# Performance work log

Measured on AMD Instinct MI355X. Metric: run time of the kernel, lower is better.

The kernel has to match this reference:

```python
import jax, jax.numpy as jnp
import numpy as np

N_EXPERTS = 32
TOPK = 256
DMODEL = 1024
EXPERT_SIZE = 2048
BATCH = 2
CUTOFF = 4096


def setup_inputs() -> dict:
    key = jax.random.key(0)
    k1, k2, k3, k4 = jax.random.split(key, 4)
    x = jax.random.normal(k1, (BATCH, CUTOFF, DMODEL), dtype=jnp.float32)
    # init scales ~ 1/sqrt(fan_in), mimicking get_init_weight
    gate = jax.random.normal(k2, (CUTOFF, N_EXPERTS), dtype=jnp.float32) / np.sqrt(DMODEL)
    lin1_weight = jax.random.normal(k3, (N_EXPERTS, DMODEL, EXPERT_SIZE), dtype=jnp.float32) / np.sqrt(DMODEL)
    lin2_weight = jax.random.normal(k4, (N_EXPERTS, EXPERT_SIZE, DMODEL), dtype=jnp.float32) / np.sqrt(EXPERT_SIZE)
    return {"x": x, "gate": gate, "lin1_weight": lin1_weight, "lin2_weight": lin2_weight}


def reference(x, gate, lin1_weight, lin2_weight):
    batch_size, cutoff, dmodel = x.shape
    n_experts = lin1_weight.shape[0]
    # gate scores: (batch, cutoff, n_experts) -> (n_experts, batch*cutoff)
    gate_out = jnp.einsum('bcd,ce->bce', x, gate)
    gate_out = jnp.transpose(gate_out, (2, 0, 1)).reshape(n_experts, batch_size * cutoff)
    probs = jax.nn.softmax(gate_out, axis=1)
    # top-k token selection per expert (computed but, faithfully to the original,
    # not used to gather tokens -- the original reshapes tokens contiguously)
    topk_values, topk_indices = jax.lax.top_k(probs, TOPK)
    # contiguous token -> expert grouping (as in the original reshape)
    xe = x.reshape(n_experts, TOPK, dmodel)  # requires batch*cutoff == n_experts*topk
    h = jax.nn.relu(jnp.einsum('ekd,eds->eks', xe, lin1_weight))
    out = jnp.einsum('eks,esd->ekd', h, lin2_weight)
    return out.reshape(batch_size, cutoff, dmodel)
```

## Files before the change

### kernel.cpp

```cpp
#include <hip/hip_runtime.h>
#include <hip/hip_bf16.h>

#define NE 32
#define MM 256
#define DM 1024
#define ES 2048

typedef __attribute__((ext_vector_type(8))) short short8;
typedef __attribute__((ext_vector_type(4))) float f32x4;
typedef unsigned int uint32;
typedef unsigned long long u64;
typedef unsigned short u16;

__device__ __forceinline__ uint32 cvt_pk_bf16(float a, float b) {
    uint32 r;
    asm("v_cvt_pk_bf16_f32 %0, %1, %2" : "=v"(r) : "v"(a), "v"(b));
    return r;
}
__device__ __forceinline__ u64 pack4(float a, float b, float c, float d) {
    return (u64)cvt_pk_bf16(a, b) | ((u64)cvt_pk_bf16(c, d) << 32);
}

__device__ __forceinline__ void gl_lds16(const void* g, void* l) {
    __builtin_amdgcn_global_load_lds(
        (const __attribute__((address_space(1))) uint32*)g,
        (__attribute__((address_space(3))) uint32*)l, 16, 0, 0);
}

__device__ __forceinline__ int b_off(int n, int k) {
    int X = ((n >> 2) & 7) ^ ((n & 3) << 1);
    return n * 128 + ((((k >> 3) ^ X) & 7) << 4) + (((k >> 2) & 1) << 3);
}

__global__ __launch_bounds__(256) void cvt_bf16(const float* __restrict__ x,
                                                u16* __restrict__ xb, int n4) {
    int i = blockIdx.x * blockDim.x + threadIdx.x;
    int stride = gridDim.x * blockDim.x;
    for (; i < n4; i += stride) {
        float4 v = ((const float4*)x)[i];
        ((u64*)xb)[i] = pack4(v.x, v.y, v.z, v.w);
    }
}

template<int N, int K, bool RELU, typename CT>
__global__ __launch_bounds__(256) void ec_gemm(
    const u16* __restrict__ A,
    const float* __restrict__ B,
    CT* __restrict__ C)
{
    constexpr int BM = 128, BN = 128, BK = 64;
    constexpr int MT = MM / BM;
    constexpr int NT = N / BN;
    constexpr int NSTEP = K / BK;
    constexpr int NP  = NE * MT;
    constexpr int PPX = NP / 8;

    int bid   = blockIdx.x;
    int xcd   = bid & 7;
    int local = bid >> 3;
    int p     = xcd * PPX + local / NT;
    int nt    = local % NT;
    int e     = p >> 1;
    int mt    = p & 1;

    const u16*   Ae = A + (size_t)(e * MM + mt * BM) * K;
    const float* Be = B + (size_t)e * K * N + (size_t)nt * BN;
    CT*          Ce = C + (size_t)(e * MM + mt * BM) * N + (size_t)nt * BN;

    __shared__ char AsB[2][BM * BK * 2];
    __shared__ char BsB[2][BN * BK * 2];

    const int t    = threadIdx.x;
    const int lane = t & 63;
    const int w    = t >> 6;
    const int wm   = (w >> 1) * 64;
    const int wn   = (w & 1) * 64;
    const int lr   = lane & 15;
    const int lg   = lane >> 4;

    const int bn4 = (t & 31) * 4;
    const int bkb = (t >> 5) * 4;

    f32x4  acc[4][4] = {};
    float4 br[2][4];

    auto gloadA = [&](int kt, int buf) {
        #pragma unroll
        for (int r = 0; r < 4; ++r) {
            int reg = w * 4 + r;
            int m   = reg * 8 + (lane >> 3);
            int s   = (lane & 7) ^ (m & 7);
            const u16* g = Ae + (size_t)m * K + kt + s * 8;
            gl_lds16(g, AsB[buf] + reg * 1024);
        }
    };
    auto loadB = [&](int kt) {
        #pragma unroll
        for (int g = 0; g < 2; ++g) {
            int k4 = g * 32 + bkb;
            const float* Bk = Be + (size_t)(kt + k4) * N + bn4;
            br[g][0] = *(const float4*)(Bk);
            br[g][1] = *(const float4*)(Bk + N);
            br[g][2] = *(const float4*)(Bk + 2 * (size_t)N);
            br[g][3] = *(const float4*)(Bk + 3 * (size_t)N);
        }
    };
    auto writeB = [&](int buf) {
        #pragma unroll
        for (int g = 0; g < 2; ++g) {
            int k4 = g * 32 + bkb;
            *(u64*)(BsB[buf] + b_off(bn4 + 0, k4)) = pack4(br[g][0].x, br[g][1].x, br[g][2].x, br[g][3].x);
            *(u64*)(BsB[buf] + b_off(bn4 + 1, k4)) = pack4(br[g][0].y, br[g][1].y, br[g][2].y, br[g][3].y);
            *(u64*)(BsB[buf] + b_off(bn4 + 2, k4)) = pack4(br[g][0].z, br[g][1].z, br[g][2].z, br[g][3].z);
            *(u64*)(BsB[buf] + b_off(bn4 + 3, k4)) = pack4(br[g][0].w, br[g][1].w, br[g][2].w, br[g][3].w);
        }
    };
    auto readA = [&](int i, int k, int buf) -> short8 {
        int m = wm + i * 16 + lr;
        int s = ((k >> 3) ^ (m & 7)) & 7;
        return *(const short8*)(AsB[buf] + m * 128 + s * 16);
    };

    loadB(0);
    gloadA(0, 0);
    writeB(0);
    __syncthreads();

    for (int ks = 0; ks < NSTEP; ++ks) {
        const int  c  = ks & 1;
        const bool pf = (ks + 1 < NSTEP);
        if (pf) { gloadA((ks + 1) * BK, c ^ 1); loadB((ks + 1) * BK); }

        #pragma unroll
        for (int kk = 0; kk < 2; ++kk) {
            int k = kk * 32 + lg * 8;
            short8 af[4], bfr[4];
            #pragma unroll
            for (int i = 0; i < 4; ++i) af[i] = readA(i, k, c);
            #pragma unroll
            for (int j = 0; j < 4; ++j)
                bfr[j] = *(const short8*)(BsB[c] + b_off(wn + j * 16 + lr, k));
            #pragma unroll
            for (int i = 0; i < 4; ++i)
                #pragma unroll
                for (int j = 0; j < 4; ++j)
                    acc[i][j] = __builtin_amdgcn_mfma_f32_16x16x32_bf16(af[i], bfr[j], acc[i][j], 0, 0, 0);
        }
        if (pf) writeB(c ^ 1);
        __syncthreads();
    }

    #pragma unroll
    for (int i = 0; i < 4; ++i) {
        #pragma unroll
        for (int rr = 0; rr < 4; ++rr) {
            int row = wm + i * 16 + lg * 4 + rr;
            CT* Cp = Ce + (size_t)row * N + wn + lr;
            if constexpr (sizeof(CT) == 2) {
                #pragma unroll
                for (int jp = 0; jp < 2; ++jp) {
                    float v0 = acc[i][2 * jp + 0][rr];
                    float v1 = acc[i][2 * jp + 1][rr];
                    if constexpr (RELU) {
                        v0 = v0 > 0.0f ? v0 : 0.0f;
                        v1 = v1 > 0.0f ? v1 : 0.0f;
                    }
                    uint32 pk = cvt_pk_bf16(v0, v1);
                    ((u16*)Cp)[(2 * jp + 0) * 16] = (u16)(pk & 0xffffu);
                    ((u16*)Cp)[(2 * jp + 1) * 16] = (u16)(pk >> 16);
                }
            } else {
                #pragma unroll
                for (int j = 0; j < 4; ++j) {
                    float v = acc[i][j][rr];
                    if constexpr (RELU) v = v > 0.0f ? v : 0.0f;
                    ((float*)Cp)[j * 16] = v;
                }
            }
        }
    }
}

extern "C" void kernel_launch(void* const* d_in, const int* in_sizes, int n_in,
                              void* d_out, int out_size, void* d_ws, size_t ws_size,
                              hipStream_t stream) {
    const float* x    = (const float*)d_in[0];
    const float* lin1 = (const float*)d_in[2];
    const float* lin2 = (const float*)d_in[3];
    float* out = (float*)d_out;

    u16* h  = (u16*)d_ws;
    u16* xb = (u16*)((char*)d_ws + (size_t)36 * 1024 * 1024);

    dim3 blk(256);
    cvt_bf16<<<2048, blk, 0, stream>>>(x, xb, NE * MM * DM / 4);
    ec_gemm<ES, DM, true,  u16  ><<<NE * (MM/128) * (ES/128), blk, 0, stream>>>(xb, lin1, h);
    ec_gemm<DM, ES, false, float><<<NE * (MM/128) * (DM/128), blk, 0, stream>>>(h, lin2, out);
}
```

Before: 181.4 us.

## Cover each expert's full 256-token tile per block so weights are read once

The GEMM block tile grows from 128 to 256 rows and 512 threads, so one workgroup covers all 256 tokens of an expert for a given column tile. Each fp32 weight tile is then loaded from global memory and converted to bf16 once instead of twice. This cuts weight traffic and conversion work, which likely dominate this bandwidth-bound kernel. In exchange it doubles LDS use for A, halves the number of blocks, and gives each thread one B row-group per k-step.

```diff
diff --git a/kernel.cpp b/kernel.cpp
--- a/kernel.cpp
+++ b/kernel.cpp
@@ -43,29 +43,25 @@
 }
 
 template<int N, int K, bool RELU, typename CT>
-__global__ __launch_bounds__(256) void ec_gemm(
+__global__ __launch_bounds__(512) void ec_gemm(
     const u16* __restrict__ A,
     const float* __restrict__ B,
     CT* __restrict__ C)
 {
-    constexpr int BM = 128, BN = 128, BK = 64;
-    constexpr int MT = MM / BM;
+    constexpr int BM = 256, BN = 128, BK = 64;
     constexpr int NT = N / BN;
     constexpr int NSTEP = K / BK;
-    constexpr int NP  = NE * MT;
-    constexpr int PPX = NP / 8;
+    constexpr int EPX = NE / 8;
 
     int bid   = blockIdx.x;
     int xcd   = bid & 7;
     int local = bid >> 3;
-    int p     = xcd * PPX + local / NT;
+    int e     = xcd * EPX + local / NT;
     int nt    = local % NT;
-    int e     = p >> 1;
-    int mt    = p & 1;
 
-    const u16*   Ae = A + (size_t)(e * MM + mt * BM) * K;
+    const u16*   Ae = A + (size_t)e * MM * K;
     const float* Be = B + (size_t)e * K * N + (size_t)nt * BN;
-    CT*          Ce = C + (size_t)(e * MM + mt * BM) * N + (size_t)nt * BN;
+    CT*          Ce = C + (size_t)e * MM * N + (size_t)nt * BN;
 
     __shared__ char AsB[2][BM * BK * 2];
     __shared__ char BsB[2][BN * BK * 2];
@@ -82,7 +78,7 @@
     const int bkb = (t >> 5) * 4;
 
     f32x4  acc[4][4] = {};
-    float4 br[2][4];
+    float4 br[4];
 
     auto gloadA = [&](int kt, int buf) {
         #pragma unroll
@@ -95,25 +91,17 @@
         }
     };
     auto loadB = [&](int kt) {
-        #pragma unroll
-        for (int g = 0; g < 2; ++g) {
-            int k4 = g * 32 + bkb;
-            const float* Bk = Be + (size_t)(kt + k4) * N + bn4;
-            br[g][0] = *(const float4*)(Bk);
-            br[g][1] = *(const float4*)(Bk + N);
-            br[g][2] = *(const float4*)(Bk + 2 * (size_t)N);
-            br[g][3] = *(const float4*)(Bk + 3 * (size_t)N);
-        }
+        const float* Bk = Be + (size_t)(kt + bkb) * N + bn4;
+        br[0] = *(const float4*)(Bk);
+        br[1] = *(const float4*)(Bk + N);
+        br[2] = *(const float4*)(Bk + 2 * (size_t)N);
+        br[3] = *(const float4*)(Bk + 3 * (size_t)N);
     };
     auto writeB = [&](int buf) {
-        #pragma unroll
-        for (int g = 0; g < 2; ++g) {
-            int k4 = g * 32 + bkb;
-            *(u64*)(BsB[buf] + b_off(bn4 + 0, k4)) = pack4(br[g][0].x, br[g][1].x, br[g][2].x, br[g][3].x);
-            *(u64*)(BsB[buf] + b_off(bn4 + 1, k4)) = pack4(br[g][0].y, br[g][1].y, br[g][2].y, br[g][3].y);
-            *(u64*)(BsB[buf] + b_off(bn4 + 2, k4)) = pack4(br[g][0].z, br[g][1].z, br[g][2].z, br[g][3].z);
-            *(u64*)(BsB[buf] + b_off(bn4 + 3, k4)) = pack4(br[g][0].w, br[g][1].w, br[g][2].w, br[g][3].w);
-        }
+        *(u64*)(BsB[buf] + b_off(bn4 + 0, bkb)) = pack4(br[0].x, br[1].x, br[2].x, br[3].x);
+        *(u64*)(BsB[buf] + b_off(bn4 + 1, bkb)) = pack4(br[0].y, br[1].y, br[2].y, br[3].y);
+        *(u64*)(BsB[buf] + b_off(bn4 + 2, bkb)) = pack4(br[0].z, br[1].z, br[2].z, br[3].z);
+        *(u64*)(BsB[buf] + b_off(bn4 + 3, bkb)) = pack4(br[0].w, br[1].w, br[2].w, br[3].w);
     };
     auto readA = [&](int i, int k, int buf) -> short8 {
         int m = wm + i * 16 + lr;
@@ -192,8 +180,7 @@
     u16* h  = (u16*)d_ws;
     u16* xb = (u16*)((char*)d_ws + (size_t)36 * 1024 * 1024);
 
-    dim3 blk(256);
-    cvt_bf16<<<2048, blk, 0, stream>>>(x, xb, NE * MM * DM / 4);
-    ec_gemm<ES, DM, true,  u16  ><<<NE * (MM/128) * (ES/128), blk, 0, stream>>>(xb, lin1, h);
-    ec_gemm<DM, ES, false, float><<<NE * (MM/128) * (DM/128), blk, 0, stream>>>(h, lin2, out);
+    cvt_bf16<<<2048, 256, 0, stream>>>(x, xb, NE * MM * DM / 4);
+    ec_gemm<ES, DM, true,  u16  ><<<NE * (ES/128), 512, 0, stream>>>(xb, lin1, h);
+    ec_gemm<DM, ES, false, float><<<NE * (DM/128), 512, 0, stream>>>(h, lin2, out);
 }
```

New measurement: 169.6 us. -6.5%, faster.
